# Kernel tuning notes

Measured on AMD Instinct MI355X. Metric: run time of the kernel, lower is better.

The kernel has to match this reference:

```python
import jax, jax.numpy as jnp
import numpy as np

B, N, D, L, H, DH, M, FF = 4, 2048, 512, 6, 8, 64, 266, 2048
EPS_LN = 1e-5
KERNEL_EPS = 1e-4


def fixed_pos_emb(n, dim):
    # performer_pytorch FixedPositionalEmbedding: cat(sin, cos) over half-dims
    inv_freq = 1.0 / (10000.0 ** (jnp.arange(0, dim, 2, dtype=jnp.float32) / dim))
    t = jnp.arange(n, dtype=jnp.float32)
    s = jnp.einsum('i,j->ij', t, inv_freq)  # [n, dim//2]
    return jnp.concatenate([jnp.sin(s), jnp.cos(s)], axis=-1)  # [n, dim]


def layer_norm(x, g, b):
    mu = x.mean(-1, keepdims=True)
    var = ((x - mu) ** 2).mean(-1, keepdims=True)
    return (x - mu) * jax.lax.rsqrt(var + EPS_LN) * g + b


def rotate_every_two(t):
    t1 = t[..., ::2]
    t2 = t[..., 1::2]
    return jnp.stack([-t2, t1], axis=-1).reshape(t.shape)


def apply_rotary(q, k, sinu):
    # sinu: [n, DH] = cat(sin_half, cos_half); repeat each value twice (interleaved)
    half = sinu.shape[-1] // 2
    sin = jnp.repeat(sinu[:, :half], 2, axis=-1)  # [n, DH]
    cos = jnp.repeat(sinu[:, half:], 2, axis=-1)
    q = q * cos + rotate_every_two(q) * sin
    k = k * cos + rotate_every_two(k) * sin
    return q, k


def softmax_kernel(data, proj, is_query):
    # data: [B,H,N,DH], proj: [M,DH]
    d = data.shape[-1]
    data_normalizer = d ** -0.25
    ratio = proj.shape[0] ** -0.5
    data_dash = jnp.einsum('bhnd,md->bhnm', data * data_normalizer, proj)
    diag = (data ** 2).sum(-1) * 0.5 * (data_normalizer ** 2)  # [B,H,N]
    if is_query:
        m = jnp.max(data_dash, axis=-1, keepdims=True)
    else:
        m = jnp.max(data_dash)
    return ratio * (jnp.exp(data_dash - diag[..., None] - m) + KERNEL_EPS)


def linear_attention(qf, kf, v):
    # qf/kf: [B,H,N,M], v: [B,H,N,DH]  (non-causal FAVOR+)
    k_sum = kf.sum(axis=-2)  # [B,H,M]
    d_inv = 1.0 / jnp.einsum('bhnm,bhm->bhn', qf, k_sum)
    context = jnp.einsum('bhnm,bhne->bhme', kf, v)  # [B,H,M,DH]
    return jnp.einsum('bhme,bhnm,bhn->bhne', context, qf, d_inv)


def setup_inputs() -> dict:
    key = jax.random.key(0)
    ks = jax.random.split(key, 8)
    std = 0.02
    inp = {
        'x': jax.random.normal(ks[0], (B, N, D), jnp.float32),
        'Wq': jax.random.normal(ks[1], (L, D, H * DH), jnp.float32) * std,
        'Wk': jax.random.normal(ks[2], (L, D, H * DH), jnp.float32) * std,
        'Wv': jax.random.normal(ks[3], (L, D, H * DH), jnp.float32) * std,
        'Wo': jax.random.normal(ks[4], (L, H * DH, D), jnp.float32) * std,
        'proj': jax.random.normal(ks[5], (L, M, DH), jnp.float32),
        'ln1_g': jnp.ones((L, D), jnp.float32),
        'ln1_b': jnp.zeros((L, D), jnp.float32),
        'W1': jax.random.normal(ks[6], (L, D, FF), jnp.float32) * std,
        'b1': jnp.zeros((L, FF), jnp.float32),
        'W2': jax.random.normal(ks[7], (L, FF, D), jnp.float32) * std,
        'b2': jnp.zeros((L, D), jnp.float32),
        'ln2_g': jnp.ones((L, D), jnp.float32),
        'ln2_b': jnp.zeros((L, D), jnp.float32),
        'lnf_g': jnp.ones((D,), jnp.float32),
        'lnf_b': jnp.zeros((D,), jnp.float32),
    }
    return inp


def reference(x, Wq, Wk, Wv, Wo, proj, ln1_g, ln1_b, W1, b1, W2, b2, ln2_g, ln2_b, lnf_g, lnf_b):
    n = x.shape[1]
    x = x + fixed_pos_emb(n, D)[None]          # additive sinusoidal emb
    sinu = fixed_pos_emb(n, DH)                 # per-head rotary table [n, DH]
    for i in range(L):
        # --- PreLayerNorm FAVOR+ self-attention ---
        h = layer_norm(x, ln1_g[i], ln1_b[i])
        q = jnp.einsum('bnd,de->bne', h, Wq[i]).reshape(B, n, H, DH).transpose(0, 2, 1, 3)
        k = jnp.einsum('bnd,de->bne', h, Wk[i]).reshape(B, n, H, DH).transpose(0, 2, 1, 3)
        v = jnp.einsum('bnd,de->bne', h, Wv[i]).reshape(B, n, H, DH).transpose(0, 2, 1, 3)
        q, k = apply_rotary(q, k, sinu)
        qf = softmax_kernel(q, proj[i], True)
        kf = softmax_kernel(k, proj[i], False)
        o = linear_attention(qf, kf, v)         # [B,H,n,DH]
        o = o.transpose(0, 2, 1, 3).reshape(B, n, H * DH)
        x = x + jnp.einsum('bne,ed->bnd', o, Wo[i])
        # --- PreLayerNorm FFN (GELU) ---
        h = layer_norm(x, ln2_g[i], ln2_b[i])
        h = jax.nn.gelu(jnp.einsum('bnd,df->bnf', h, W1[i]) + b1[i], approximate=False)
        x = x + jnp.einsum('bnf,fd->bnd', h, W2[i]) + b2[i]
    return layer_norm(x, lnf_g, lnf_b)
```

## Files before the change

kernel.cpp:

```cpp
#include <hip/hip_runtime.h>
#include <hip/hip_bf16.h>
#include <cstdint>

typedef float v4f __attribute__((ext_vector_type(4)));
typedef short v8s __attribute__((ext_vector_type(8)));
typedef unsigned short u16;

#define N_SEQ 2048
#define D_MODEL 512
#define N_LAYER 6
#define N_HEAD 8
#define D_HEAD 64
#define M_FEAT 266
#define M_PAD 288
#define M_ALLOC 384
#define FF_DIM 2048
#define BATCH 4
#define ROWS 8192
#define BHN 65536

__device__ __forceinline__ float b2f(u16 u) {
  return __uint_as_float(((uint32_t)u) << 16);
}
__device__ __forceinline__ u16 f2b(float f) {
  union { __hip_bfloat16 h; u16 u; } c;
  c.h = __float2bfloat16(f);
  return c.u;
}
__device__ __forceinline__ float wave_sum(float v) {
#pragma unroll
  for (int o = 1; o < 64; o <<= 1) v += __shfl_xor(v, o);
  return v;
}
__device__ __forceinline__ float wave_max(float v) {
#pragma unroll
  for (int o = 1; o < 64; o <<= 1) v = fmaxf(v, __shfl_xor(v, o));
  return v;
}

__device__ __forceinline__ void mfma_bf16(v4f& d, v8s a, v8s b) {
  asm volatile("v_mfma_f32_16x16x32_bf16 %0, %1, %2, %0" : "+v"(d) : "v"(a), "v"(b));
}

__device__ __forceinline__ void async16(const u16* g, u16* l) {
  __builtin_amdgcn_global_load_lds(
      (const __attribute__((address_space(1))) uint32_t*)g,
      (__attribute__((address_space(3))) uint32_t*)l, 16, 0, 0);
}

template <int EPI, int KSPLIT>
__global__ void __launch_bounds__(512, 2)
gemm3s(const u16* __restrict__ A, const u16* __restrict__ B,
       void* __restrict__ Cv, const float* __restrict__ bias,
       int K, int ldc)
{
  extern __shared__ u16 lds[];
  const int t = threadIdx.x;
  const int lane = t & 63;
  const int w = t >> 6;
  const int wm = w >> 2;
  const int wn = w & 3;
  const int tiM = blockIdx.x << 7, tiN = blockIdx.y << 8;
  const int ks = (KSPLIT > 1) ? blockIdx.z : 0;
  const int kchunk = K / KSPLIT;
  const int NT = kchunk >> 6;

  const int rr = lane & 15;
  const int kq = (lane >> 4) << 3;
  const int swz = (rr & 7) << 3;
  const int c0 = kq ^ swz;
  const int c1 = (32 + kq) ^ swz;

  const int prow = t >> 3;
  const int scol = (((t & 7) ^ (prow & 7)) << 3);
  const u16* Abase = A + (long long)(tiM + prow) * K + scol + (long long)ks * kchunk;
  const u16* Bbase = B + (long long)(tiN + prow) * K + scol + (long long)ks * kchunk;
  const long long r64 = 64LL * K;

  v4f acc[4][4] = {};

  auto stageA = [&](int s, int kt) {
    const u16* src = Abase + (long long)kt * 64;
    u16* dst = &lds[s * 24576 + t * 8];
    async16(src, dst);
    async16(src + r64, dst + 4096);
  };
  auto stageB1 = [&](int s, int kt, int j) {
    async16(Bbase + (long long)kt * 64 + (long long)j * r64,
            &lds[s * 24576 + 8192 + j * 4096 + t * 8]);
  };

  stageA(0, 0);
#pragma unroll
  for (int j = 0; j < 4; j++) stageB1(0, 0, j);
  stageA(1, 1);
#pragma unroll
  for (int j = 0; j < 4; j++) stageB1(1, 1, j);
  asm volatile("s_waitcnt vmcnt(6)" ::: "memory");
  __builtin_amdgcn_s_barrier();

  for (int kt = 0; kt < NT; ++kt) {
    const int s = kt % 3;
    const int sp = (kt + 2) % 3;
    const bool st = (kt + 2 < NT);
    const int ab = s * 24576;
    const int bb = ab + 8192;
    v8s af[4], bf[4];

#pragma unroll
    for (int i = 0; i < 4; i++) af[i] = *(const v8s*)&lds[ab + (wm * 64 + i * 16 + rr) * 64 + c0];
#pragma unroll
    for (int i = 0; i < 4; i++) bf[i] = *(const v8s*)&lds[bb + (wn * 64 + i * 16 + rr) * 64 + c0];
    if (st) { stageA(sp, kt + 2); stageB1(sp, kt + 2, 0); }
    __builtin_amdgcn_s_barrier();
    __builtin_amdgcn_s_setprio(1);
#pragma unroll
    for (int m = 0; m < 4; m++)
#pragma unroll
      for (int n = 0; n < 4; n++) mfma_bf16(acc[m][n], af[m], bf[n]);
    __builtin_amdgcn_s_setprio(0);
    __builtin_amdgcn_s_barrier();

#pragma unroll
    for (int i = 0; i < 4; i++) af[i] = *(const v8s*)&lds[ab + (wm * 64 + i * 16 + rr) * 64 + c1];
#pragma unroll
    for (int i = 0; i < 4; i++) bf[i] = *(const v8s*)&lds[bb + (wn * 64 + i * 16 + rr) * 64 + c1];
    if (st) { stageB1(sp, kt + 2, 1); stageB1(sp, kt + 2, 2); stageB1(sp, kt + 2, 3); }
    __builtin_amdgcn_s_barrier();
    __builtin_amdgcn_s_setprio(1);
#pragma unroll
    for (int m = 0; m < 4; m++)
#pragma unroll
      for (int n = 0; n < 4; n++) mfma_bf16(acc[m][n], af[m], bf[n]);
    __builtin_amdgcn_s_setprio(0);
    if (st) asm volatile("s_waitcnt vmcnt(6)" ::: "memory");
    else    asm volatile("s_waitcnt vmcnt(0)" ::: "memory");
    __builtin_amdgcn_s_barrier();
  }

  __builtin_amdgcn_sched_barrier(0);
  asm volatile("s_nop 7\ns_nop 7\ns_nop 7");
  __builtin_amdgcn_sched_barrier(0);

  const int r4 = (lane >> 4) << 2;
  const int cc = lane & 15;
#pragma unroll
  for (int mf = 0; mf < 4; mf++)
#pragma unroll
    for (int nf = 0; nf < 4; nf++)
#pragma unroll
      for (int i = 0; i < 4; i++) {
        int row = tiM + wm * 64 + mf * 16 + r4 + i;
        int col = tiN + wn * 64 + nf * 16 + cc;
        float v = acc[mf][nf][i];
        if (EPI == 0) {
          ((u16*)Cv)[(long long)row * ldc + col] = f2b(v);
        } else if (EPI == 3) {
          float hv = v + bias[col];
          float gg = 0.5f * hv * (1.0f + erff(hv * 0.70710678118f));
          ((u16*)Cv)[(long long)row * ldc + col] = f2b(gg);
        } else {
          ((float*)Cv)[((long long)ks * ROWS + row) * ldc + col] = v;
        }
      }
}

__global__ void ff2red(const float* __restrict__ part, const float* __restrict__ bias,
                       float* __restrict__ x)
{
  long long i = ((long long)blockIdx.x * 256 + threadIdx.x) * 8;
  int col = (int)(i & 511);
  v4f s0 = {}, s1 = {};
#pragma unroll
  for (int ks = 0; ks < 2; ks++) {
    const float* p = part + (long long)ks * (ROWS * 512LL) + i;
    s0 += *(const v4f*)p;
    s1 += *(const v4f*)(p + 4);
  }
  v4f b0 = *(const v4f*)(bias + col);
  v4f b1 = *(const v4f*)(bias + col + 4);
  v4f x0 = *(const v4f*)(x + i), x1 = *(const v4f*)(x + i + 4);
  x0 += s0 + b0;
  x1 += s1 + b1;
  *(v4f*)(x + i) = x0;
  *(v4f*)(x + i + 4) = x1;
}

template <int EPI, int BN, int KSPLIT>
__global__ void __launch_bounds__(256, 4)
gemm2(const u16* __restrict__ A, const u16* __restrict__ B,
      void* __restrict__ Cv, const float* __restrict__ bias,
      int K, int ldc, long long sA, long long sB, long long sC,
      float scale, int Ncap, int Mcap, unsigned int* __restrict__ gmax)
{
  __shared__ u16 As[2][128 * 32];
  __shared__ u16 Bs[2][BN * 32];
  __shared__ float smax[4];
  const int zz = blockIdx.z;
  const int z = (KSPLIT > 1) ? zz / KSPLIT : zz;
  const int ks = (KSPLIT > 1) ? zz % KSPLIT : 0;
  const int kchunk = K / KSPLIT;
  const u16* Ag = A + (long long)z * sA + ks * kchunk;
  const u16* Bg = B + (long long)z * sB + ks * kchunk;
  const int t = threadIdx.x;
  const int lane = t & 63;
  const int w = t >> 6;
  constexpr int NF = BN / 32;
  const int wm = (w >> 1) << 6;
  const int wn = (w & 1) * (BN / 2);
  const int tiM = blockIdx.x << 7, tiN = blockIdx.y * BN;

  const int srow = t >> 2;
  const int scol = (t & 3) << 3;
  const u16* Ap = Ag + (long long)(tiM + srow) * K + scol;
  const u16* Bp = Bg + (long long)(tiN + srow) * K + scol;
  const long long rstride = 64LL * K;

  const int rr = lane & 15;
  const int kc = (lane >> 4) << 3;

  v4f acc[4][NF] = {};

  const int nk = kchunk >> 5;
  auto stage = [&](int buf, int k0) {
    async16(Ap + k0, &As[buf][t * 8]);
    async16(Ap + k0 + rstride, &As[buf][t * 8 + 2048]);
    async16(Bp + k0, &Bs[buf][t * 8]);
    if (BN == 128) async16(Bp + k0 + rstride, &Bs[buf][t * 8 + 2048]);
  };

  stage(0, 0);
  __syncthreads();
  int cur = 0;
  for (int kt = 0; kt < nk; ++kt) {
    if (kt + 1 < nk) stage(cur ^ 1, (kt + 1) << 5);
    v8s af[4], bf[NF];
#pragma unroll
    for (int i = 0; i < 4; i++) af[i] = *(const v8s*)&As[cur][(wm + rr + i * 16) * 32 + kc];
#pragma unroll
    for (int i = 0; i < NF; i++) bf[i] = *(const v8s*)&Bs[cur][(wn + rr + i * 16) * 32 + kc];
#pragma unroll
    for (int fm = 0; fm < 4; fm++)
#pragma unroll
      for (int fn = 0; fn < NF; fn++)
        mfma_bf16(acc[fm][fn], af[fm], bf[fn]);
    __syncthreads();
    cur ^= 1;
  }

  __builtin_amdgcn_sched_barrier(0);
  asm volatile("s_nop 7\ns_nop 7\ns_nop 7");
  __builtin_amdgcn_sched_barrier(0);

  const int r4 = (lane >> 4) << 2;
  const int cc = lane & 15;
  float lmax = -3e38f;
#pragma unroll
  for (int fm = 0; fm < 4; fm++)
#pragma unroll
    for (int fn = 0; fn < NF; fn++)
#pragma unroll
      for (int i = 0; i < 4; i++) {
        int row = tiM + wm + fm * 16 + r4 + i;
        int col = tiN + wn + fn * 16 + cc;
        float v = acc[fm][fn][i];
        if (EPI == 5) {
          if (row < Mcap && col < Ncap)
            ((float*)Cv)[((long long)zz * M_ALLOC + row) * 64 + col] = v;
        } else if (EPI == 6) {
          float sv = v * scale;
          if (col < Ncap) ((float*)Cv)[(long long)row * ldc + col] = sv;
          if (col < M_FEAT) lmax = fmaxf(lmax, sv);
        }
      }

  if (EPI == 6) {
    lmax = wave_max(lmax);
    if (lane == 0) smax[w] = lmax;
    __syncthreads();
    if (t == 0) {
      float m = fmaxf(fmaxf(smax[0], smax[1]), fmaxf(smax[2], smax[3]));
      unsigned int u = __float_as_uint(m);
      unsigned int key = (u & 0x80000000u) ? ~u : (u | 0x80000000u);
      atomicMax(gmax, key);
    }
  }
}

template <int EPI>
__global__ void __launch_bounds__(256, 6)
gemm_small(const u16* __restrict__ A, const u16* __restrict__ B,
           void* __restrict__ Cv, const float* __restrict__ bias,
           int K, int ldc, long long sA, long long sB)
{
  __shared__ u16 As[2][64 * 32];
  __shared__ u16 Bs[2][64 * 32];
  const int z = blockIdx.z;
  const u16* Ag = A + (long long)z * sA;
  const u16* Bg = B + (long long)z * sB;
  const int t = threadIdx.x;
  const int lane = t & 63;
  const int w = t >> 6;
  const int wm = (w >> 1) << 5;
  const int wn = (w & 1) << 5;
  const int tiM = blockIdx.x << 6, tiN = blockIdx.y << 6;

  const int srow = t >> 2;
  const int scol = (t & 3) << 3;
  const u16* Ap = Ag + (long long)(tiM + srow) * K + scol;
  const u16* Bp = Bg + (long long)(tiN + srow) * K + scol;

  const int rr = lane & 15;
  const int kc = (lane >> 4) << 3;

  v4f acc[2][2] = {};

  const int nk = K >> 5;
  auto stage = [&](int buf, int k0) {
    async16(Ap + k0, &As[buf][t * 8]);
    async16(Bp + k0, &Bs[buf][t * 8]);
  };

  stage(0, 0);
  __syncthreads();
  int cur = 0;
  for (int kt = 0; kt < nk; ++kt) {
    if (kt + 1 < nk) stage(cur ^ 1, (kt + 1) << 5);
    v8s af[2], bf[2];
#pragma unroll
    for (int i = 0; i < 2; i++) af[i] = *(const v8s*)&As[cur][(wm + rr + i * 16) * 32 + kc];
#pragma unroll
    for (int i = 0; i < 2; i++) bf[i] = *(const v8s*)&Bs[cur][(wn + rr + i * 16) * 32 + kc];
#pragma unroll
    for (int fm = 0; fm < 2; fm++)
#pragma unroll
      for (int fn = 0; fn < 2; fn++)
        mfma_bf16(acc[fm][fn], af[fm], bf[fn]);
    __syncthreads();
    cur ^= 1;
  }

  __builtin_amdgcn_sched_barrier(0);
  asm volatile("s_nop 7\ns_nop 7\ns_nop 7");
  __builtin_amdgcn_sched_barrier(0);

  const int r4 = (lane >> 4) << 2;
  const int cc = lane & 15;
#pragma unroll
  for (int fm = 0; fm < 2; fm++)
#pragma unroll
    for (int fn = 0; fn < 2; fn++)
#pragma unroll
      for (int i = 0; i < 4; i++) {
        int row = tiM + wm + fm * 16 + r4 + i;
        int col = tiN + wn + fn * 16 + cc;
        float v = acc[fm][fn][i];
        if (EPI == 0) {
          ((u16*)Cv)[(long long)row * ldc + col] = f2b(v);
        } else if (EPI == 2) {
          long long idx = (long long)row * ldc + col;
          float bb = bias ? bias[col] : 0.0f;
          ((float*)Cv)[idx] += v + bb;
        } else if (EPI == 3) {
          float hv = v + bias[col];
          float gg = 0.5f * hv * (1.0f + erff(hv * 0.70710678118f));
          ((u16*)Cv)[(long long)row * ldc + col] = f2b(gg);
        } else {
          int b_ = z >> 3, h_ = z & 7;
          ((u16*)Cv)[(long long)(b_ * N_SEQ + row) * 512 + h_ * 64 + col] = f2b(v);
        }
      }
}

__global__ void __launch_bounds__(384, 3)
ddq_qf(const u16* __restrict__ qr, const u16* __restrict__ proj,
       const float* __restrict__ diag, const float* __restrict__ ksum,
       u16* __restrict__ qf)
{
  __shared__ u16 As[2][64 * 32];
  __shared__ u16 Bs[2][288 * 32];
  __shared__ float redw[6][64];
  __shared__ float rowv[64];
  __shared__ float sdg[64];
  const int bh = blockIdx.z;
  const int tiM = blockIdx.x << 6;
  const int t = threadIdx.x;
  const int lane = t & 63;
  const int w = t >> 6;
  const u16* Ag = qr + (long long)bh * (N_SEQ * 64);
  const int srow = t >> 2, scol = (t & 3) << 3;
  const u16* Ap = Ag + (long long)(tiM + srow) * 64 + scol;
  const int rr = lane & 15, kc = (lane >> 4) << 3;
  const int wn = w * 48;

  if (t < 64) sdg[t] = diag[(long long)bh * N_SEQ + tiM + t];

  v4f acc[4][3] = {};
  auto stage = [&](int buf, int k0) {
    if (t < 256) async16(Ap + k0, &As[buf][t * 8]);
#pragma unroll
    for (int j = 0; j < 3; j++) {
      int idx = j * 384 + t;
      async16(proj + (long long)(idx >> 2) * 64 + ((idx & 3) << 3) + k0,
              &Bs[buf][j * 3072 + t * 8]);
    }
  };

  stage(0, 0);
  __syncthreads();
  for (int kt = 0; kt < 2; ++kt) {
    if (kt == 0) stage(1, 32);
    v8s af[4], bf[3];
#pragma unroll
    for (int i = 0; i < 4; i++) af[i] = *(const v8s*)&As[kt][(rr + i * 16) * 32 + kc];
#pragma unroll
    for (int i = 0; i < 3; i++) bf[i] = *(const v8s*)&Bs[kt][(wn + i * 16 + rr) * 32 + kc];
#pragma unroll
    for (int fm = 0; fm < 4; fm++)
#pragma unroll
      for (int fn = 0; fn < 3; fn++)
        mfma_bf16(acc[fm][fn], af[fm], bf[fn]);
    __syncthreads();
  }

  __builtin_amdgcn_sched_barrier(0);
  asm volatile("s_nop 7\ns_nop 7\ns_nop 7");
  __builtin_amdgcn_sched_barrier(0);

  const int r4 = (lane >> 4) << 2;
  const int cc = lane & 15;
  const float sc = 0.35355339f;

#pragma unroll
  for (int fm = 0; fm < 4; fm++)
#pragma unroll
    for (int i = 0; i < 4; i++) {
      float m = -3e38f;
#pragma unroll
      for (int fn = 0; fn < 3; fn++) {
        int col = wn + fn * 16 + cc;
        float v = acc[fm][fn][i] * sc;
        if (col < M_FEAT) m = fmaxf(m, v);
      }
#pragma unroll
      for (int o = 1; o < 16; o <<= 1) m = fmaxf(m, __shfl_xor(m, o));
      if (cc == 0) redw[w][fm * 16 + r4 + i] = m;
    }
  __syncthreads();
  if (t < 64) {
    float g = redw[0][t];
#pragma unroll
    for (int ww = 1; ww < 6; ww++) g = fmaxf(g, redw[ww][t]);
    rowv[t] = g;
  }
  __syncthreads();

  float ksv[3];
#pragma unroll
  for (int fn = 0; fn < 3; fn++) ksv[fn] = ksum[bh * M_PAD + wn + fn * 16 + cc];

#pragma unroll
  for (int fm = 0; fm < 4; fm++)
#pragma unroll
    for (int i = 0; i < 4; i++) {
      int row = fm * 16 + r4 + i;
      float gm = rowv[row];
      float dg = sdg[row];
      float s = 0.0f;
#pragma unroll
      for (int fn = 0; fn < 3; fn++) {
        float e = 0.06131389f * (expf(acc[fm][fn][i] * sc - dg - gm) + 1e-4f);
        acc[fm][fn][i] = e;
        s += e * ksv[fn];
      }
#pragma unroll
      for (int o = 1; o < 16; o <<= 1) s += __shfl_xor(s, o);
      if (cc == 0) redw[w][row] = s;
    }
  __syncthreads();
  if (t < 64) {
    float s = redw[0][t];
#pragma unroll
    for (int ww = 1; ww < 6; ww++) s += redw[ww][t];
    rowv[t] = 1.0f / s;
  }
  __syncthreads();

#pragma unroll
  for (int fm = 0; fm < 4; fm++)
#pragma unroll
    for (int i = 0; i < 4; i++) {
      int row = fm * 16 + r4 + i;
      float dinv = rowv[row];
#pragma unroll
      for (int fn = 0; fn < 3; fn++) {
        int col = wn + fn * 16 + cc;
        qf[((long long)bh * N_SEQ + tiM + row) * M_PAD + col] =
            f2b(acc[fm][fn][i] * dinv);
      }
    }
}

template <bool F32OUT>
__global__ void ln_kernel(const float* __restrict__ x, const float* __restrict__ g,
                          const float* __restrict__ b, void* __restrict__ out)
{
  const int row = blockIdx.x * 4 + (threadIdx.x >> 6);
  const int lane = threadIdx.x & 63;
  const float* xr = x + (long long)row * D_MODEL + lane * 8;
  v4f v0 = *(const v4f*)xr;
  v4f v1 = *(const v4f*)(xr + 4);
  float s = v0[0] + v0[1] + v0[2] + v0[3] + v1[0] + v1[1] + v1[2] + v1[3];
  float sq = v0[0]*v0[0] + v0[1]*v0[1] + v0[2]*v0[2] + v0[3]*v0[3]
           + v1[0]*v1[0] + v1[1]*v1[1] + v1[2]*v1[2] + v1[3]*v1[3];
  s = wave_sum(s);
  sq = wave_sum(sq);
  float mu = s * (1.0f / D_MODEL);
  float var = sq * (1.0f / D_MODEL) - mu * mu;
  float rstd = rsqrtf(var + 1e-5f);
  v4f g0 = *(const v4f*)(g + lane * 8), g1 = *(const v4f*)(g + lane * 8 + 4);
  v4f bb0 = *(const v4f*)(b + lane * 8), bb1 = *(const v4f*)(b + lane * 8 + 4);
  float y[8];
#pragma unroll
  for (int j = 0; j < 4; j++) y[j] = (v0[j] - mu) * rstd * g0[j] + bb0[j];
#pragma unroll
  for (int j = 0; j < 4; j++) y[4 + j] = (v1[j] - mu) * rstd * g1[j] + bb1[j];
  if (F32OUT) {
    float* op = (float*)out + (long long)row * D_MODEL + lane * 8;
    v4f o0 = {y[0], y[1], y[2], y[3]}, o1 = {y[4], y[5], y[6], y[7]};
    *(v4f*)op = o0;
    *(v4f*)(op + 4) = o1;
  } else {
    u16* op = (u16*)out + (long long)row * D_MODEL + lane * 8;
    alignas(16) u16 tmp[8];
#pragma unroll
    for (int j = 0; j < 8; j++) tmp[j] = f2b(y[j]);
    *(v8s*)op = *(v8s*)tmp;
  }
}

__global__ void posadd(const float* __restrict__ xin, float* __restrict__ x)
{
  long long i = (long long)blockIdx.x * 256 + threadIdx.x;
  int d = (int)(i & 511);
  int n = (int)((i >> 9) & 2047);
  int j = d & 255;
  float sarg = (float)n * expf(-0.035977892f * (float)j);
  float pe = (d < 256) ? sinf(sarg) : cosf(sarg);
  x[i] = xin[i] + pe;
}

__global__ void rotab(float* __restrict__ ts, float* __restrict__ tc)
{
  int i = blockIdx.x * 64 + threadIdx.x;
  int n = i >> 5, j = i & 31;
  float sarg = (float)n * expf(-0.28782314f * (float)j);
  float s, c;
  sincosf(sarg, &s, &c);
  ts[i] = s;
  tc[i] = c;
}

__global__ void rotary_kernel(const u16* __restrict__ qkv,
                              const float* __restrict__ ts, const float* __restrict__ tc,
                              u16* __restrict__ qr, u16* __restrict__ kr,
                              float* __restrict__ dq, float* __restrict__ dk)
{
  int bid = blockIdx.x * 4 + (threadIdx.x >> 6);
  int n = bid & 2047;
  int h = (bid >> 11) & 7;
  int b = bid >> 14;
  int lane = threadIdx.x & 63;
  long long src = ((long long)(b * N_SEQ + n)) * 1536 + h * 64 + lane;
  float qv = b2f(qkv[src]);
  float kv = b2f(qkv[src + 512]);
  int j = lane >> 1;
  float sn = ts[n * 32 + j], cn = tc[n * 32 + j];
  float qp = __shfl_xor(qv, 1), kp = __shfl_xor(kv, 1);
  float qrv = (lane & 1) ? (qv * cn + qp * sn) : (qv * cn - qp * sn);
  float krv = (lane & 1) ? (kv * cn + kp * sn) : (kv * cn - kp * sn);
  u16 qb = f2b(qrv), kb = f2b(krv);
  long long dst = ((long long)bid) * 64 + lane;
  qr[dst] = qb;
  kr[dst] = kb;
  float q2 = b2f(qb); q2 *= q2;
  float k2 = b2f(kb); k2 *= k2;
  q2 = wave_sum(q2);
  k2 = wave_sum(k2);
  if (lane == 0) { dq[bid] = q2 * 0.0625f; dk[bid] = k2 * 0.0625f; }
}

__global__ void vtrans(const u16* __restrict__ qkv, u16* __restrict__ vT)
{
  int bid = blockIdx.x;
  int nt = bid & 31;
  int h = (bid >> 5) & 7;
  int b = bid >> 8;
  __shared__ u16 st[64][72];
  int t = threadIdx.x;
  int r = t >> 2, c = (t & 3) << 4;
  long long src = ((long long)(b * N_SEQ + nt * 64 + r)) * 1536 + 1024 + h * 64 + c;
  *(v8s*)&st[r][c] = *(const v8s*)(qkv + src);
  *(v8s*)&st[r][c + 8] = *(const v8s*)(qkv + src + 8);
  __syncthreads();
  alignas(16) u16 tmp[16];
#pragma unroll
  for (int jj = 0; jj < 16; jj++) tmp[jj] = st[c + jj][r];
  long long dst = ((long long)((b * 8 + h) * 64 + r)) * N_SEQ + nt * 64 + c;
  *(v8s*)(vT + dst) = *(v8s*)&tmp[0];
  *(v8s*)(vT + dst + 8) = *(v8s*)&tmp[8];
}

__global__ void wtrans(const float* __restrict__ src, u16* __restrict__ dst,
                       int Ks, int Ns, long long sSrc, long long sDst)
{
  int l = blockIdx.z;
  src += (long long)l * sSrc;
  dst += (long long)l * sDst;
  int n0 = blockIdx.x << 6, k0 = blockIdx.y << 6;
  __shared__ float st[64][68];
  int t = threadIdx.x;
  int r = t >> 2, c = (t & 3) << 4;
  const float* sp = src + (long long)(k0 + r) * Ns + n0 + c;
#pragma unroll
  for (int jj = 0; jj < 16; jj += 4) *(v4f*)&st[r][c + jj] = *(const v4f*)(sp + jj);
  __syncthreads();
  alignas(16) u16 tmp[16];
#pragma unroll
  for (int jj = 0; jj < 16; jj++) tmp[jj] = f2b(st[c + jj][r]);
  u16* dp = dst + (long long)(n0 + r) * Ks + k0 + c;
  *(v8s*)(dp) = *(v8s*)&tmp[0];
  *(v8s*)(dp + 8) = *(v8s*)&tmp[8];
}

__global__ void projconv(const float* __restrict__ proj, u16* __restrict__ out)
{
  int i = blockIdx.x * 256 + threadIdx.x;
  int dh = i & 63;
  int m = (i >> 6) % M_ALLOC;
  int l = i / (M_ALLOC * 64);
  float v = (m < M_FEAT) ? proj[((long long)l * M_FEAT + m) * 64 + dh] : 0.0f;
  out[i] = f2b(v);
}

__global__ void resetmax(unsigned int* p) { *p = 0u; }

__global__ void kfprep(const float* __restrict__ dd, const float* __restrict__ diag,
                       const unsigned int* __restrict__ kmax,
                       u16* __restrict__ kfT, float* __restrict__ part)
{
  int ntile = blockIdx.x;
  int m0 = blockIdx.y << 6;
  int bh = blockIdx.z;
  int n0 = ntile << 6;
  __shared__ float st[64][65];
  unsigned int kk = kmax[0];
  float km = (kk & 0x80000000u) ? __uint_as_float(kk ^ 0x80000000u)
                                : __uint_as_float(~kk);
  int t = threadIdx.x;
  int r = t >> 2, c = (t & 3) << 4;
  const float* dp = dd + ((long long)bh * N_SEQ + n0 + r) * M_PAD + m0 + c;
  float dg = diag[(long long)bh * N_SEQ + n0 + r];
  float vals[16];
  if (m0 + c + 16 <= M_PAD) {
#pragma unroll
    for (int j = 0; j < 16; j += 4) *(v4f*)&vals[j] = *(const v4f*)(dp + j);
  } else {
#pragma unroll
    for (int j = 0; j < 16; j++) vals[j] = (m0 + c + j < M_PAD) ? dp[j] : 0.0f;
  }
#pragma unroll
  for (int j = 0; j < 16; j++) {
    int m = m0 + c + j;
    float e = (m < M_FEAT) ? 0.06131389f * (expf(vals[j] - dg - km) + 1e-4f) : 0.0f;
    st[r][c + j] = e;
  }
  __syncthreads();
  int mr = t >> 2, nc = (t & 3) << 4;
  float s = 0.0f;
  alignas(16) u16 tmp[16];
#pragma unroll
  for (int j = 0; j < 16; j++) {
    float e = st[nc + j][mr];
    s += e;
    tmp[j] = f2b(e);
  }
  s += __shfl_xor(s, 1);
  s += __shfl_xor(s, 2);
  int m = m0 + mr;
  if (m < M_PAD) {
    u16* op = kfT + ((long long)bh * M_ALLOC + m) * N_SEQ + n0 + nc;
    *(v8s*)op = *(v8s*)&tmp[0];
    *(v8s*)(op + 8) = *(v8s*)&tmp[8];
    if ((t & 3) == 0)
      part[((long long)bh * M_PAD + m) * 32 + ntile] = s;
  }
}

__global__ void ksumred(const float* __restrict__ part, float* __restrict__ ksum)
{
  int i = blockIdx.x * 256 + threadIdx.x;
  if (i >= 32 * M_PAD) return;
  const float* p = part + (long long)i * 32;
  float s = 0.0f;
#pragma unroll
  for (int j = 0; j < 32; j += 4) {
    v4f v = *(const v4f*)(p + j);
    s += v[0] + v[1] + v[2] + v[3];
  }
  ksum[i] = s;
}

__global__ void ctxred(const float* __restrict__ part, u16* __restrict__ ctxT)
{
  int bh = blockIdx.y;
  int m0 = blockIdx.x << 6;
  __shared__ float st[64][65];
  int t = threadIdx.x;
  int r = t >> 2, c = (t & 3) << 4;
  int m = m0 + r;
  v4f s[4] = {};
  if (m < M_PAD) {
    for (int ks = 0; ks < 8; ks++) {
      const float* p = part + (((long long)bh * 8 + ks) * M_ALLOC + m) * 64 + c;
#pragma unroll
      for (int j = 0; j < 4; j++) s[j] += *(const v4f*)(p + j * 4);
    }
  }
#pragma unroll
  for (int j = 0; j < 4; j++)
#pragma unroll
    for (int e = 0; e < 4; e++) st[r][c + j * 4 + e] = s[j][e];
  __syncthreads();
  int e = t >> 2, mc = (t & 3) << 4;
  if (m0 + mc < M_PAD) {
    alignas(16) u16 tmp[16];
#pragma unroll
    for (int j = 0; j < 16; j++) tmp[j] = f2b(st[mc + j][e]);
    u16* op = ctxT + ((long long)bh * 64 + e) * M_PAD + m0 + mc;
    *(v8s*)op = *(v8s*)&tmp[0];
    *(v8s*)(op + 8) = *(v8s*)&tmp[8];
  }
}

extern "C" void kernel_launch(void* const* d_in, const int* in_sizes, int n_in,
                              void* d_out, int out_size, void* d_ws, size_t ws_size,
                              hipStream_t stream)
{
  const float* x_in = (const float*)d_in[0];
  const float* Wq  = (const float*)d_in[1];
  const float* Wk  = (const float*)d_in[2];
  const float* Wv  = (const float*)d_in[3];
  const float* Wo  = (const float*)d_in[4];
  const float* Pr  = (const float*)d_in[5];
  const float* ln1g = (const float*)d_in[6];
  const float* ln1b = (const float*)d_in[7];
  const float* W1  = (const float*)d_in[8];
  const float* b1  = (const float*)d_in[9];
  const float* W2  = (const float*)d_in[10];
  const float* b2  = (const float*)d_in[11];
  const float* ln2g = (const float*)d_in[12];
  const float* ln2b = (const float*)d_in[13];
  const float* lnfg = (const float*)d_in[14];
  const float* lnfb = (const float*)d_in[15];

  hipFuncSetAttribute(reinterpret_cast<const void*>(&gemm3s<0, 1>),
                      hipFuncAttributeMaxDynamicSharedMemorySize, 147456);
  hipFuncSetAttribute(reinterpret_cast<const void*>(&gemm3s<3, 1>),
                      hipFuncAttributeMaxDynamicSharedMemorySize, 147456);
  hipFuncSetAttribute(reinterpret_cast<const void*>(&gemm3s<5, 2>),
                      hipFuncAttributeMaxDynamicSharedMemorySize, 147456);

  char* ws = (char*)d_ws;
  size_t off = 0;
  auto alloc = [&](size_t bytes) -> void* {
    void* p = ws + off;
    off = (off + bytes + 255) & ~(size_t)255;
    return p;
  };

  float* x      = (float*)alloc((size_t)ROWS * D_MODEL * 4);
  float* tsin   = (float*)alloc((size_t)N_SEQ * 32 * 4);
  float* tcos   = (float*)alloc((size_t)N_SEQ * 32 * 4);
  u16*   wqkvT  = (u16*)alloc((size_t)N_LAYER * 1536 * 512 * 2);
  u16*   woT    = (u16*)alloc((size_t)N_LAYER * 512 * 512 * 2);
  u16*   w1T    = (u16*)alloc((size_t)N_LAYER * 2048 * 512 * 2);
  u16*   w2T    = (u16*)alloc((size_t)N_LAYER * 512 * 2048 * 2);
  u16*   projT  = (u16*)alloc((size_t)N_LAYER * M_ALLOC * 64 * 2);
  u16*   hbuf   = (u16*)alloc((size_t)ROWS * D_MODEL * 2);
  u16*   obuf   = (u16*)alloc((size_t)ROWS * D_MODEL * 2);
  float* big    = (float*)alloc((size_t)32 * N_SEQ * M_PAD * 4);
  u16*   qrbuf  = (u16*)alloc((size_t)BHN * 64 * 2);
  u16*   krbuf  = (u16*)alloc((size_t)BHN * 64 * 2);
  u16*   vTbuf  = (u16*)alloc((size_t)BHN * 64 * 2);
  float* diagq  = (float*)alloc((size_t)BHN * 4);
  float* diagk  = (float*)alloc((size_t)BHN * 4);
  unsigned int* kmaxu = (unsigned int*)alloc(256);
  u16*   kfT    = (u16*)alloc((size_t)32 * M_ALLOC * N_SEQ * 2);
  float* part   = (float*)alloc((size_t)32 * 8 * M_ALLOC * 64 * 4);
  float* kspart = (float*)alloc((size_t)32 * M_PAD * 32 * 4);
  u16*   ctxT   = (u16*)alloc((size_t)32 * 64 * M_PAD * 2);
  float* ksum   = (float*)alloc((size_t)32 * M_PAD * 4);
  (void)alloc(1 << 20);
  (void)ws_size; (void)in_sizes; (void)n_in; (void)out_size;
  float* ff2part = (float*)kfT;

  posadd<<<16384, 256, 0, stream>>>(x_in, x);
  rotab<<<1024, 64, 0, stream>>>(tsin, tcos);
  wtrans<<<dim3(8, 8, 6), 256, 0, stream>>>(Wq, wqkvT, 512, 512, 512LL * 512, 1536LL * 512);
  wtrans<<<dim3(8, 8, 6), 256, 0, stream>>>(Wk, wqkvT + 512LL * 512, 512, 512, 512LL * 512, 1536LL * 512);
  wtrans<<<dim3(8, 8, 6), 256, 0, stream>>>(Wv, wqkvT + 1024LL * 512, 512, 512, 512LL * 512, 1536LL * 512);
  wtrans<<<dim3(8, 8, 6), 256, 0, stream>>>(Wo, woT, 512, 512, 512LL * 512, 512LL * 512);
  wtrans<<<dim3(32, 8, 6), 256, 0, stream>>>(W1, w1T, 512, 2048, 512LL * 2048, 2048LL * 512);
  wtrans<<<dim3(8, 32, 6), 256, 0, stream>>>(W2, w2T, 2048, 512, 2048LL * 512, 512LL * 2048);
  projconv<<<(N_LAYER * M_ALLOC * 64) / 256, 256, 0, stream>>>(Pr, projT);

  for (int l = 0; l < N_LAYER; l++) {
    const u16* wq = wqkvT + (long long)l * 1536 * 512;
    const u16* wo = woT + (long long)l * 512 * 512;
    const u16* w1 = w1T + (long long)l * 2048 * 512;
    const u16* w2 = w2T + (long long)l * 512 * 2048;
    const u16* pj = projT + (long long)l * M_ALLOC * 64;

    resetmax<<<1, 1, 0, stream>>>(kmaxu);
    ln_kernel<false><<<ROWS / 4, 256, 0, stream>>>(x, ln1g + l * 512, ln1b + l * 512, hbuf);
    gemm3s<0, 1><<<dim3(64, 6), 512, 147456, stream>>>(hbuf, wq, big, nullptr, 512, 1536);
    rotary_kernel<<<BHN / 4, 256, 0, stream>>>((u16*)big, tsin, tcos, qrbuf, krbuf, diagq, diagk);
    vtrans<<<1024, 256, 0, stream>>>((u16*)big, vTbuf);
    gemm2<6, 128, 1><<<dim3(512, 3, 1), 256, 0, stream>>>(krbuf, pj, big, nullptr,
        64, M_PAD, 0, 0, 0, 0.35355339f, M_PAD, BHN, kmaxu);
    kfprep<<<dim3(32, 5, 32), 256, 0, stream>>>(big, diagk, kmaxu, kfT, kspart);
    ksumred<<<(32 * M_PAD + 255) / 256, 256, 0, stream>>>(kspart, ksum);
    gemm2<5, 64, 8><<<dim3(3, 1, 256), 256, 0, stream>>>(kfT, vTbuf, part, nullptr,
        2048, 64, (long long)M_ALLOC * N_SEQ, 64LL * N_SEQ, 0, 1.0f, 64, M_PAD, nullptr);
    ctxred<<<dim3(5, 32), 256, 0, stream>>>(part, ctxT);
    ddq_qf<<<dim3(32, 1, 32), 384, 0, stream>>>(qrbuf, pj, diagq, ksum, kfT);
    gemm_small<4><<<dim3(32, 1, 32), 256, 0, stream>>>(kfT, ctxT, obuf, nullptr,
        M_PAD, 0, (long long)N_SEQ * M_PAD, 64LL * M_PAD);
    gemm_small<2><<<dim3(128, 8, 1), 256, 0, stream>>>(obuf, wo, x, nullptr,
        512, 512, 0, 0);
    ln_kernel<false><<<ROWS / 4, 256, 0, stream>>>(x, ln2g + l * 512, ln2b + l * 512, hbuf);
    gemm3s<3, 1><<<dim3(64, 8), 512, 147456, stream>>>(hbuf, w1, big, b1 + (long long)l * 2048,
        512, 2048);
    gemm3s<5, 2><<<dim3(64, 2, 2), 512, 147456, stream>>>((u16*)big, w2, ff2part, nullptr,
        2048, 512);
    ff2red<<<2048, 256, 0, stream>>>(ff2part, b2 + (long long)l * 512, x);
  }

  ln_kernel<true><<<ROWS / 4, 256, 0, stream>>>(x, lnfg, lnfb, d_out);
}
```

Measured before the change: 1.584 ms.

## Merge GEMM K-half phases into one barrier step and use polynomial GELU

The 3-stage GEMM main loop used to split each 64-wide K tile into two half-steps, each with its own LDS reads, staged loads and barriers. Now it reads both halves of the A and B fragments at once, issues all six async loads for stage kt+2 together, and runs the 32 MFMAs back to back, so only one barrier remains per K tile. This cuts barrier and sync overhead but raises register pressure, which may matter under the (512, 2) launch bounds. Separately, the exact erff GELU in the epilogues is replaced by the Abramowitz-Stegun polynomial erf using a fast reciprocal and exp, which is cheaper but slightly less accurate.

```diff
diff --git a/kernel.cpp b/kernel.cpp
--- a/kernel.cpp
+++ b/kernel.cpp
@@ -38,6 +38,16 @@
   return v;
 }
 
+__device__ __forceinline__ float gelu_f(float x) {
+  float ax = fabsf(x) * 0.70710678118f;
+  float tt = __builtin_amdgcn_rcpf(fmaf(0.3275911f, ax, 1.0f));
+  float poly = tt * fmaf(tt, fmaf(tt, fmaf(tt, fmaf(tt, 1.061405429f, -1.453152027f),
+                                           1.421413741f), -0.284496736f), 0.254829592f);
+  float er = 1.0f - poly * __expf(-ax * ax);
+  er = copysignf(er, x);
+  return 0.5f * x * (1.0f + er);
+}
+
 __device__ __forceinline__ void mfma_bf16(v4f& d, v8s a, v8s b) {
   asm volatile("v_mfma_f32_16x16x32_bf16 %0, %1, %2, %0" : "+v"(d) : "v"(a), "v"(b));
 }
@@ -79,23 +89,19 @@
 
   v4f acc[4][4] = {};
 
-  auto stageA = [&](int s, int kt) {
-    const u16* src = Abase + (long long)kt * 64;
-    u16* dst = &lds[s * 24576 + t * 8];
-    async16(src, dst);
-    async16(src + r64, dst + 4096);
+  auto stage6 = [&](int s, int kt) {
+    const u16* sa = Abase + (long long)kt * 64;
+    u16* da = &lds[s * 24576 + t * 8];
+    async16(sa, da);
+    async16(sa + r64, da + 4096);
+    const u16* sb = Bbase + (long long)kt * 64;
+    u16* db = &lds[s * 24576 + 8192 + t * 8];
+#pragma unroll
+    for (int j = 0; j < 4; j++) async16(sb + (long long)j * r64, db + j * 4096);
   };
-  auto stageB1 = [&](int s, int kt, int j) {
-    async16(Bbase + (long long)kt * 64 + (long long)j * r64,
-            &lds[s * 24576 + 8192 + j * 4096 + t * 8]);
-  };
-
-  stageA(0, 0);
-#pragma unroll
-  for (int j = 0; j < 4; j++) stageB1(0, 0, j);
-  stageA(1, 1);
-#pragma unroll
-  for (int j = 0; j < 4; j++) stageB1(1, 1, j);
+
+  stage6(0, 0);
+  stage6(1, 1);
   asm volatile("s_waitcnt vmcnt(6)" ::: "memory");
   __builtin_amdgcn_s_barrier();
 
@@ -105,33 +111,23 @@
     const bool st = (kt + 2 < NT);
     const int ab = s * 24576;
     const int bb = ab + 8192;
-    v8s af[4], bf[4];
-
-#pragma unroll
-    for (int i = 0; i < 4; i++) af[i] = *(const v8s*)&lds[ab + (wm * 64 + i * 16 + rr) * 64 + c0];
-#pragma unroll
-    for (int i = 0; i < 4; i++) bf[i] = *(const v8s*)&lds[bb + (wn * 64 + i * 16 + rr) * 64 + c0];
-    if (st) { stageA(sp, kt + 2); stageB1(sp, kt + 2, 0); }
-    __builtin_amdgcn_s_barrier();
+    v8s a0[4], a1[4], b0[4], b1[4];
+#pragma unroll
+    for (int i = 0; i < 4; i++) {
+      a0[i] = *(const v8s*)&lds[ab + (wm * 64 + i * 16 + rr) * 64 + c0];
+      a1[i] = *(const v8s*)&lds[ab + (wm * 64 + i * 16 + rr) * 64 + c1];
+      b0[i] = *(const v8s*)&lds[bb + (wn * 64 + i * 16 + rr) * 64 + c0];
+      b1[i] = *(const v8s*)&lds[bb + (wn * 64 + i * 16 + rr) * 64 + c1];
+    }
+    if (st) stage6(sp, kt + 2);
     __builtin_amdgcn_s_setprio(1);
 #pragma unroll
     for (int m = 0; m < 4; m++)
 #pragma unroll
-      for (int n = 0; n < 4; n++) mfma_bf16(acc[m][n], af[m], bf[n]);
-    __builtin_amdgcn_s_setprio(0);
-    __builtin_amdgcn_s_barrier();
-
-#pragma unroll
-    for (int i = 0; i < 4; i++) af[i] = *(const v8s*)&lds[ab + (wm * 64 + i * 16 + rr) * 64 + c1];
-#pragma unroll
-    for (int i = 0; i < 4; i++) bf[i] = *(const v8s*)&lds[bb + (wn * 64 + i * 16 + rr) * 64 + c1];
-    if (st) { stageB1(sp, kt + 2, 1); stageB1(sp, kt + 2, 2); stageB1(sp, kt + 2, 3); }
-    __builtin_amdgcn_s_barrier();
-    __builtin_amdgcn_s_setprio(1);
-#pragma unroll
-    for (int m = 0; m < 4; m++)
-#pragma unroll
-      for (int n = 0; n < 4; n++) mfma_bf16(acc[m][n], af[m], bf[n]);
+      for (int n = 0; n < 4; n++) {
+        mfma_bf16(acc[m][n], a0[m], b0[n]);
+        mfma_bf16(acc[m][n], a1[m], b1[n]);
+      }
     __builtin_amdgcn_s_setprio(0);
     if (st) asm volatile("s_waitcnt vmcnt(6)" ::: "memory");
     else    asm volatile("s_waitcnt vmcnt(0)" ::: "memory");
@@ -156,9 +152,7 @@
         if (EPI == 0) {
           ((u16*)Cv)[(long long)row * ldc + col] = f2b(v);
         } else if (EPI == 3) {
-          float hv = v + bias[col];
-          float gg = 0.5f * hv * (1.0f + erff(hv * 0.70710678118f));
-          ((u16*)Cv)[(long long)row * ldc + col] = f2b(gg);
+          ((u16*)Cv)[(long long)row * ldc + col] = f2b(gelu_f(v + bias[col]));
         } else {
           ((float*)Cv)[((long long)ks * ROWS + row) * ldc + col] = v;
         }
@@ -362,9 +356,7 @@
           float bb = bias ? bias[col] : 0.0f;
           ((float*)Cv)[idx] += v + bb;
         } else if (EPI == 3) {
-          float hv = v + bias[col];
-          float gg = 0.5f * hv * (1.0f + erff(hv * 0.70710678118f));
-          ((u16*)Cv)[(long long)row * ldc + col] = f2b(gg);
+          ((u16*)Cv)[(long long)row * ldc + col] = f2b(gelu_f(v + bias[col]));
         } else {
           int b_ = z >> 3, h_ = z & 7;
           ((u16*)Cv)[(long long)(b_ * N_SEQ + row) * 512 + h_ * 64 + col] = f2b(v);
```

After: 1.526 ms. -3.7%, faster.
